# Kernel optimization log

Measured on AMD Instinct MI355X. Metric: run time of the kernel, lower is better.

Reference implementation:

```python
import jax, jax.numpy as jnp
import numpy as np

T, H, E, F = 2048, 1024, 32, 512   # tokens, hidden, routed experts, moe intermediate
K, NG, TG = 8, 8, 4                # top_k, n_group, topk_group
FS = 1024                          # shared-expert intermediate = n_shared(2) * F
SCALE = 2.5                        # routed_scaling_factor


def _silu_and_mul(gu):
    g, u = jnp.split(gu, 2, axis=-1)
    return jax.nn.silu(g) * u


def _route(x, gate_w, bias):
    # DeepSeek-V3 noaux_tc grouped top-k with correction bias (sigmoid scores)
    logits = x @ gate_w.T                                   # [T,E]
    scores = jax.nn.sigmoid(logits.astype(jnp.float32))
    sc = scores + bias[None, :]                             # biased scores, selection only
    n_tok = sc.shape[0]
    grp = sc.reshape(n_tok, NG, E // NG)
    top2, _ = jax.lax.top_k(grp, 2)
    group_scores = top2.sum(-1)                             # [T,NG]
    _, gidx = jax.lax.top_k(group_scores, TG)
    gmask = jnp.zeros((n_tok, NG), scores.dtype).at[jnp.arange(n_tok)[:, None], gidx].set(1.0)
    emask = jnp.repeat(gmask, E // NG, axis=1)              # [T,E]
    masked = jnp.where(emask > 0, sc, -jnp.inf)
    _, topk_idx = jax.lax.top_k(masked, K)                  # [T,K]
    w = jnp.take_along_axis(scores, topk_idx, axis=1)       # unbiased scores as weights
    w = w / (w.sum(-1, keepdims=True) + 1e-20)              # renormalize (norm_topk_prob)
    return w, topk_idx


def _forward(x, gate_w, corr_bias, w_gate_up, w_down, shared_gate_up, shared_down):
    w, idx = _route(x, gate_w, corr_bias)
    # dense grouped-GEMM reference: every expert on every token, sparse combine
    gu = jnp.einsum('th,egh->teg', x, w_gate_up)            # [T,E,2F]
    h = _silu_and_mul(gu)                                   # [T,E,F]
    y = jnp.einsum('tef,ehf->teh', h, w_down)               # [T,E,H]
    n_tok = x.shape[0]
    combine = jnp.zeros((n_tok, E), x.dtype).at[jnp.arange(n_tok)[:, None], idx].add(w.astype(x.dtype))
    routed = jnp.einsum('te,teh->th', combine, y) * SCALE
    shared = _silu_and_mul(x @ shared_gate_up.T) @ shared_down.T
    return routed + shared


def setup_inputs() -> dict:
    key = jax.random.key(0)
    ks = jax.random.split(key, 7)
    return {
        "hidden_states": jax.random.normal(ks[0], (T, H), jnp.float32),
        "gate_w": jax.random.normal(ks[1], (E, H), jnp.float32) * 0.02,
        "corr_bias": jax.random.normal(ks[2], (E,), jnp.float32) * 0.01,
        "w_gate_up": jax.random.normal(ks[3], (E, 2 * F, H), jnp.float32) * 0.02,
        "w_down": jax.random.normal(ks[4], (E, H, F), jnp.float32) * 0.02,
        "shared_gate_up": jax.random.normal(ks[5], (2 * FS, H), jnp.float32) * 0.02,
        "shared_down": jax.random.normal(ks[6], (H, FS), jnp.float32) * 0.02,
        "num_global_tokens": T,
        "max_num_tokens_per_gpu": T,
    }


def reference(hidden_states, gate_w, corr_bias, w_gate_up, w_down, shared_gate_up, shared_down, num_global_tokens, max_num_tokens_per_gpu):
    return _forward(hidden_states, gate_w, corr_bias, w_gate_up, w_down, shared_gate_up, shared_down)
```

## Files before the change

### kernel.cpp

```cpp
#include <hip/hip_runtime.h>
#include <hip/hip_bf16.h>

#define T_TOK 2048
#define H_DIM 1024
#define E_EXP 32
#define F_DIM 512
#define FS_DIM 1024
#define K_TOP 8
#define NGRP 8
#define TGRP 4
#define GSZ (E_EXP / NGRP)
#define RSCALE 2.5f
#define CAP 2048

typedef short  short8 __attribute__((ext_vector_type(8)));
typedef __bf16 bf16x4 __attribute__((ext_vector_type(4)));
typedef __bf16 bf16x8 __attribute__((ext_vector_type(8)));
typedef float  f32x4  __attribute__((ext_vector_type(4)));

#define NROUTE_BLK (T_TOK / 4)
__global__ __launch_bounds__(256) void prep_kernel(
    const float* __restrict__ x, const float* __restrict__ gw,
    const float* __restrict__ bias, int* __restrict__ tk_idx,
    float* __restrict__ tk_w, __bf16* __restrict__ xb,
    const float* __restrict__ s0, __bf16* __restrict__ d0, int n0,
    const float* __restrict__ s1, __bf16* __restrict__ d1, int n1,
    const float* __restrict__ s2, __bf16* __restrict__ d2, int n2,
    const float* __restrict__ s3, __bf16* __restrict__ d3, int n3) {
  if (blockIdx.x < NROUTE_BLK) {
    const int wid = threadIdx.x >> 6, lane = threadIdx.x & 63;
    const int t = blockIdx.x * 4 + wid;
    float xr[16];
#pragma unroll
    for (int i = 0; i < 16; i++) xr[i] = x[t * H_DIM + i * 64 + lane];
#pragma unroll
    for (int i = 0; i < 16; i++) xb[t * H_DIM + i * 64 + lane] = (__bf16)xr[i];
    float sc[E_EXP];
#pragma unroll
    for (int e = 0; e < E_EXP; e++) {
      const float* w = gw + e * H_DIM;
      float s = 0.f;
#pragma unroll
      for (int i = 0; i < 16; i++) s += xr[i] * w[i * 64 + lane];
#pragma unroll
      for (int off = 32; off > 0; off >>= 1) s += __shfl_xor(s, off);
      sc[e] = 1.f / (1.f + expf(-s));
    }
    if (lane == 0) {
      float b[E_EXP];
      for (int e = 0; e < E_EXP; e++) b[e] = sc[e] + bias[e];
      float gs[NGRP];
      for (int g = 0; g < NGRP; g++) {
        float m1 = -1e30f, m2 = -1e30f;
        for (int j = 0; j < GSZ; j++) {
          float v = b[g * GSZ + j];
          if (v > m1) { m2 = m1; m1 = v; } else if (v > m2) { m2 = v; }
        }
        gs[g] = m1 + m2;
      }
      unsigned gmask = 0;
      for (int it = 0; it < TGRP; it++) {
        float best = -1e30f; int bi = 0;
        for (int g = 0; g < NGRP; g++)
          if (!((gmask >> g) & 1) && gs[g] > best) { best = gs[g]; bi = g; }
        gmask |= 1u << bi;
      }
      unsigned emask = 0; float wsum = 0.f;
      int idx8[K_TOP];
      for (int it = 0; it < K_TOP; it++) {
        float best = -1e30f; int bi = 0;
        for (int e = 0; e < E_EXP; e++) {
          if (!((gmask >> (e / GSZ)) & 1)) continue;
          if ((emask >> e) & 1) continue;
          if (b[e] > best) { best = b[e]; bi = e; }
        }
        emask |= 1u << bi;
        idx8[it] = bi;
        wsum += sc[bi];
      }
      const float inv = 1.f / (wsum + 1e-20f);
      for (int k = 0; k < K_TOP; k++) {
        tk_idx[t * K_TOP + k] = idx8[k];
        tk_w[t * K_TOP + k] = sc[idx8[k]] * inv;
      }
    }
  } else {
    const int ntot8 = (n0 + n1 + n2 + n3) >> 1;
    const int nthr = (gridDim.x - NROUTE_BLK) * 256;
    int gid = (blockIdx.x - NROUTE_BLK) * 256 + threadIdx.x;
    for (; gid < ntot8; gid += nthr) {
      int t = gid << 1;
      const float* src; __bf16* dst;
      if (t < n0) { src = s0; dst = d0; }
      else { t -= n0;
        if (t < n1) { src = s1; dst = d1; }
        else { t -= n1;
          if (t < n2) { src = s2; dst = d2; }
          else { t -= n2; src = s3; dst = d3; }
        }
      }
      const float4 va = reinterpret_cast<const float4*>(src)[t];
      const float4 vb = reinterpret_cast<const float4*>(src)[t + 1];
      bf16x8 o;
      o[0] = (__bf16)va.x; o[1] = (__bf16)va.y; o[2] = (__bf16)va.z; o[3] = (__bf16)va.w;
      o[4] = (__bf16)vb.x; o[5] = (__bf16)vb.y; o[6] = (__bf16)vb.z; o[7] = (__bf16)vb.w;
      *reinterpret_cast<bf16x8*>(reinterpret_cast<bf16x4*>(dst) + t) = o;
    }
  }
}

__global__ void scatter_kernel(const int* __restrict__ tk_idx, int* __restrict__ counts,
                               int* __restrict__ recs) {
  const int i = blockIdx.x * blockDim.x + threadIdx.x;
  if (i >= T_TOK * K_TOP) return;
  const int e = tk_idx[i];
  const int pos = atomicAdd(&counts[e], 1);
  recs[e * CAP + pos] = i;
}

#define BM 128
#define BN 128
#define BK 64

__device__ __forceinline__ void gload_lds16(const void* g, void* l) {
  __builtin_amdgcn_global_load_lds(
      (__attribute__((address_space(1))) const void*)g,
      (__attribute__((address_space(3))) void*)l, 16, 0, 0);
}

template <int PHASE>
__global__ __launch_bounds__(256) void gemm_fused(
    const __bf16* __restrict__ Ar, const __bf16* __restrict__ As_,
    const __bf16* __restrict__ Br, const __bf16* __restrict__ Bs_,
    void* __restrict__ OutR, void* __restrict__ OutS,
    const int* __restrict__ recs, const int* __restrict__ counts,
    const float* __restrict__ tk_w) {

  const int z = blockIdx.z;
  const bool routed = (z < E_EXP);
  const int e = z;
  const int m0 = blockIdx.y * BM;
  const int bx = blockIdx.x;

  int count = T_TOK, off_e = 0;
  if (routed) {
    count = counts[e];
    for (int i = 0; i < E_EXP; i++) off_e += (i < e) ? counts[i] : 0;
    if (m0 >= count) return;
  }
  const int K = (PHASE == 0) ? H_DIM : (routed ? F_DIM : FS_DIM);

  const int tid = threadIdx.x, wid = tid >> 6, lane = tid & 63;

  __shared__ __align__(16) __bf16 Atile[BM * BK];
  __shared__ __align__(16) __bf16 Btile[BN * BK];

  const int colk = (lane & 7) * 8;
  const __bf16* aptr[4];
  const __bf16* bptr[4];
#pragma unroll
  for (int i = 0; i < 4; i++) {
    const int row = wid * 32 + i * 8 + (lane >> 3);
    int r = m0 + row; if (r > count - 1) r = count - 1;
    if (PHASE == 0) {
      if (routed) {
        const int rec = recs[e * CAP + r];
        aptr[i] = Ar + (size_t)(rec >> 3) * H_DIM + colk;
      } else {
        aptr[i] = As_ + (size_t)r * H_DIM + colk;
      }
    } else {
      if (routed) aptr[i] = Ar + (size_t)(off_e + r) * F_DIM + colk;
      else        aptr[i] = As_ + (size_t)r * FS_DIM + colk;
    }
    if (PHASE == 0) {
      if (routed) {
        const int brow = (row < 64) ? (bx * 64 + row) : (F_DIM + bx * 64 + row - 64);
        bptr[i] = Br + (size_t)e * 2 * F_DIM * H_DIM + (size_t)brow * H_DIM + colk;
      } else {
        const int s = z - E_EXP;
        const int fglob = s * 512 + bx * 64 + (row & 63);
        const int brow = (row < 64) ? fglob : (FS_DIM + fglob);
        bptr[i] = Bs_ + (size_t)brow * H_DIM + colk;
      }
    } else {
      if (routed) {
        const int brow = bx * BN + row;
        bptr[i] = Br + (size_t)e * H_DIM * F_DIM + (size_t)brow * F_DIM + colk;
      } else {
        const int brow = bx * BN + row;
        bptr[i] = Bs_ + (size_t)brow * FS_DIM + colk;
      }
    }
  }

  f32x4 acc[2][8];
#pragma unroll
  for (int a = 0; a < 2; a++)
#pragma unroll
    for (int b = 0; b < 8; b++) acc[a][b] = f32x4{0.f, 0.f, 0.f, 0.f};

  const int lr = lane & 15, lh = lane >> 4;

  for (int k0 = 0; k0 < K; k0 += BK) {
#pragma unroll
    for (int i = 0; i < 4; i++)
      gload_lds16(aptr[i] + k0, (char*)Atile + (wid * 4 + i) * 1024);
#pragma unroll
    for (int i = 0; i < 4; i++)
      gload_lds16(bptr[i] + k0, (char*)Btile + (wid * 4 + i) * 1024);
    __syncthreads();
#pragma unroll
    for (int kk = 0; kk < 2; kk++) {
      short8 af[2], bfr[8];
#pragma unroll
      for (int fm = 0; fm < 2; fm++)
        af[fm] = *reinterpret_cast<const short8*>(&Atile[(wid * 32 + fm * 16 + lr) * BK + kk * 32 + lh * 8]);
#pragma unroll
      for (int fn = 0; fn < 8; fn++)
        bfr[fn] = *reinterpret_cast<const short8*>(&Btile[(fn * 16 + lr) * BK + kk * 32 + lh * 8]);
#pragma unroll
      for (int fn = 0; fn < 8; fn++)
#pragma unroll
        for (int fm = 0; fm < 2; fm++)
          acc[fm][fn] = __builtin_amdgcn_mfma_f32_16x16x32_bf16(af[fm], bfr[fn], acc[fm][fn], 0, 0, 0);
    }
    __syncthreads();
  }

  if (PHASE == 0) {
#pragma unroll
    for (int fm = 0; fm < 2; fm++)
#pragma unroll
      for (int j = 0; j < 4; j++) {
        const int row = wid * 32 + fm * 16 + lh * 4 + j;
        if (m0 + row < count) {
#pragma unroll
          for (int fn = 0; fn < 4; fn++) {
            const float g = acc[fm][fn][j], u = acc[fm][fn + 4][j];
            const float hv = g / (1.f + expf(-g)) * u;
            if (routed) {
              const int f = bx * 64 + fn * 16 + lr;
              ((__bf16*)OutR)[(size_t)(off_e + m0 + row) * F_DIM + f] = (__bf16)hv;
            } else {
              const int s = z - E_EXP;
              const int f = s * 512 + bx * 64 + fn * 16 + lr;
              ((__bf16*)OutS)[(size_t)(m0 + row) * FS_DIM + f] = (__bf16)hv;
            }
          }
        }
      }
  } else {
#pragma unroll
    for (int fm = 0; fm < 2; fm++)
#pragma unroll
      for (int j = 0; j < 4; j++) {
        const int row = wid * 32 + fm * 16 + lh * 4 + j;
        if (m0 + row < count) {
          if (routed) {
            const int rec = recs[e * CAP + m0 + row];
            const float w = tk_w[rec];
            const size_t base = (size_t)rec * H_DIM + bx * BN;
#pragma unroll
            for (int fn = 0; fn < 8; fn++)
              ((float*)OutR)[base + fn * 16 + lr] = acc[fm][fn][j] * w;
          } else {
#pragma unroll
            for (int fn = 0; fn < 8; fn++)
              ((float*)OutS)[(size_t)(m0 + row) * H_DIM + bx * BN + fn * 16 + lr] = acc[fm][fn][j];
          }
        }
      }
  }
}

__global__ void combine_kernel(const float* __restrict__ y_slot, float* __restrict__ out) {
  const int gid = blockIdx.x * blockDim.x + threadIdx.x;
  const int t = gid >> 8;
  const int c0 = (gid & 255) * 4;
  float4 s = {0.f, 0.f, 0.f, 0.f};
#pragma unroll
  for (int k = 0; k < K_TOP; k++) {
    const float4 v = *reinterpret_cast<const float4*>(&y_slot[((size_t)t * K_TOP + k) * H_DIM + c0]);
    s.x += v.x; s.y += v.y; s.z += v.z; s.w += v.w;
  }
  float4 o = *reinterpret_cast<float4*>(&out[(size_t)t * H_DIM + c0]);
  o.x += RSCALE * s.x; o.y += RSCALE * s.y; o.z += RSCALE * s.z; o.w += RSCALE * s.w;
  *reinterpret_cast<float4*>(&out[(size_t)t * H_DIM + c0]) = o;
}

extern "C" void kernel_launch(void* const* d_in, const int* in_sizes, int n_in,
                              void* d_out, int out_size, void* d_ws, size_t ws_size,
                              hipStream_t stream) {
  const float* x    = (const float*)d_in[0];
  const float* gw   = (const float*)d_in[1];
  const float* bias = (const float*)d_in[2];
  const float* wgu  = (const float*)d_in[3];
  const float* wd   = (const float*)d_in[4];
  const float* sgu  = (const float*)d_in[5];
  const float* sd   = (const float*)d_in[6];

  char* ws = (char*)d_ws;
  size_t o = 0;
  auto alloc = [&](size_t bytes) {
    char* p = ws + o;
    o += (bytes + 255) & ~(size_t)255;
    return (void*)p;
  };
  __bf16* xb     = (__bf16*)alloc((size_t)T_TOK * H_DIM * 2);
  __bf16* wgub   = (__bf16*)alloc((size_t)E_EXP * 2 * F_DIM * H_DIM * 2);
  __bf16* wdb    = (__bf16*)alloc((size_t)E_EXP * H_DIM * F_DIM * 2);
  __bf16* sgub   = (__bf16*)alloc((size_t)2 * FS_DIM * H_DIM * 2);
  __bf16* sdb    = (__bf16*)alloc((size_t)H_DIM * FS_DIM * 2);
  __bf16* h_buf  = (__bf16*)alloc((size_t)T_TOK * K_TOP * F_DIM * 2);
  float*  y_slot = (float*) alloc((size_t)T_TOK * K_TOP * H_DIM * 4);
  __bf16* hs     = (__bf16*)alloc((size_t)T_TOK * FS_DIM * 2);
  int*   tk_idx  = (int*)  alloc((size_t)T_TOK * K_TOP * 4);
  float* tk_w    = (float*)alloc((size_t)T_TOK * K_TOP * 4);
  int*   counts  = (int*)  alloc((size_t)E_EXP * 4);
  int*   recs    = (int*)  alloc((size_t)E_EXP * CAP * 4);
  if (o > ws_size) return;

  hipMemsetAsync(counts, 0, E_EXP * 4, stream);
  prep_kernel<<<2048, 256, 0, stream>>>(
      x, gw, bias, tk_idx, tk_w, xb,
      wgu, wgub, E_EXP * 2 * F_DIM * H_DIM / 4,
      wd,  wdb,  E_EXP * H_DIM * F_DIM / 4,
      sgu, sgub, 2 * FS_DIM * H_DIM / 4,
      sd,  sdb,  H_DIM * FS_DIM / 4);

  scatter_kernel<<<(T_TOK * K_TOP + 255) / 256, 256, 0, stream>>>(tk_idx, counts, recs);

  gemm_fused<0><<<dim3(F_DIM / 64, T_TOK / BM, E_EXP + 2), 256, 0, stream>>>(
      xb, xb, wgub, sgub, h_buf, hs, recs, counts, tk_w);

  gemm_fused<1><<<dim3(H_DIM / BN, T_TOK / BM, E_EXP + 1), 256, 0, stream>>>(
      h_buf, hs, wdb, sdb, y_slot, d_out, recs, counts, tk_w);

  combine_kernel<<<T_TOK * H_DIM / 4 / 256, 256, 0, stream>>>(y_slot, (float*)d_out);
}
```

Before: 290.3 us.

## Overlap down-proj weight conversion with gate-up GEMM via extra grid slices

Moves the fp32-to-bf16 conversion of the routed and shared down-projection weights out of the prep kernel and into extra z-slices of the phase-0 gate/up GEMM launch. The prep kernel then converts only the gate/up weights, and the down-weight conversion runs alongside the GEMM tiles. This is meant to hide part of the bandwidth-bound conversion behind compute-bound GEMM work. In exchange, the two workloads now compete for memory bandwidth and CUs inside the GEMM launch, and the outcome depends on how blocks are scheduled.

```diff
diff --git a/kernel.cpp b/kernel.cpp
--- a/kernel.cpp
+++ b/kernel.cpp
@@ -12,11 +12,30 @@
 #define GSZ (E_EXP / NGRP)
 #define RSCALE 2.5f
 #define CAP 2048
+#define NCVT_SLICE 8
 
 typedef short  short8 __attribute__((ext_vector_type(8)));
 typedef __bf16 bf16x4 __attribute__((ext_vector_type(4)));
 typedef __bf16 bf16x8 __attribute__((ext_vector_type(8)));
 typedef float  f32x4  __attribute__((ext_vector_type(4)));
+
+__device__ __forceinline__ void cvt8_range(const float* __restrict__ s0, __bf16* __restrict__ d0, int n0,
+                                           const float* __restrict__ s1, __bf16* __restrict__ d1, int n1,
+                                           int base, int nthr) {
+  const int ntot8 = (n0 + n1) >> 1;
+  for (int gid = base; gid < ntot8; gid += nthr) {
+    int t = gid << 1;
+    const float* src; __bf16* dst;
+    if (t < n0) { src = s0; dst = d0; }
+    else { t -= n0; src = s1; dst = d1; }
+    const float4 va = reinterpret_cast<const float4*>(src)[t];
+    const float4 vb = reinterpret_cast<const float4*>(src)[t + 1];
+    bf16x8 o;
+    o[0] = (__bf16)va.x; o[1] = (__bf16)va.y; o[2] = (__bf16)va.z; o[3] = (__bf16)va.w;
+    o[4] = (__bf16)vb.x; o[5] = (__bf16)vb.y; o[6] = (__bf16)vb.z; o[7] = (__bf16)vb.w;
+    *reinterpret_cast<bf16x8*>(reinterpret_cast<bf16x4*>(dst) + t) = o;
+  }
+}
 
 #define NROUTE_BLK (T_TOK / 4)
 __global__ __launch_bounds__(256) void prep_kernel(
@@ -24,9 +43,7 @@
     const float* __restrict__ bias, int* __restrict__ tk_idx,
     float* __restrict__ tk_w, __bf16* __restrict__ xb,
     const float* __restrict__ s0, __bf16* __restrict__ d0, int n0,
-    const float* __restrict__ s1, __bf16* __restrict__ d1, int n1,
-    const float* __restrict__ s2, __bf16* __restrict__ d2, int n2,
-    const float* __restrict__ s3, __bf16* __restrict__ d3, int n3) {
+    const float* __restrict__ s1, __bf16* __restrict__ d1, int n1) {
   if (blockIdx.x < NROUTE_BLK) {
     const int wid = threadIdx.x >> 6, lane = threadIdx.x & 63;
     const int t = blockIdx.x * 4 + wid;
@@ -85,27 +102,9 @@
       }
     }
   } else {
-    const int ntot8 = (n0 + n1 + n2 + n3) >> 1;
     const int nthr = (gridDim.x - NROUTE_BLK) * 256;
-    int gid = (blockIdx.x - NROUTE_BLK) * 256 + threadIdx.x;
-    for (; gid < ntot8; gid += nthr) {
-      int t = gid << 1;
-      const float* src; __bf16* dst;
-      if (t < n0) { src = s0; dst = d0; }
-      else { t -= n0;
-        if (t < n1) { src = s1; dst = d1; }
-        else { t -= n1;
-          if (t < n2) { src = s2; dst = d2; }
-          else { t -= n2; src = s3; dst = d3; }
-        }
-      }
-      const float4 va = reinterpret_cast<const float4*>(src)[t];
-      const float4 vb = reinterpret_cast<const float4*>(src)[t + 1];
-      bf16x8 o;
-      o[0] = (__bf16)va.x; o[1] = (__bf16)va.y; o[2] = (__bf16)va.z; o[3] = (__bf16)va.w;
-      o[4] = (__bf16)vb.x; o[5] = (__bf16)vb.y; o[6] = (__bf16)vb.z; o[7] = (__bf16)vb.w;
-      *reinterpret_cast<bf16x8*>(reinterpret_cast<bf16x4*>(dst) + t) = o;
-    }
+    const int base = (blockIdx.x - NROUTE_BLK) * 256 + threadIdx.x;
+    cvt8_range(s0, d0, n0, s1, d1, n1, base, nthr);
   }
 }
 
@@ -134,9 +133,19 @@
     const __bf16* __restrict__ Br, const __bf16* __restrict__ Bs_,
     void* __restrict__ OutR, void* __restrict__ OutS,
     const int* __restrict__ recs, const int* __restrict__ counts,
-    const float* __restrict__ tk_w) {
+    const float* __restrict__ tk_w,
+    const float* __restrict__ cvt_s0, __bf16* __restrict__ cvt_d0, int cvt_n0,
+    const float* __restrict__ cvt_s1, __bf16* __restrict__ cvt_d1, int cvt_n1) {
 
   const int z = blockIdx.z;
+
+  if (PHASE == 0 && z >= E_EXP + 2) {
+    const int nblk = NCVT_SLICE * gridDim.x * gridDim.y;
+    const int bid = (z - (E_EXP + 2)) * gridDim.x * gridDim.y + blockIdx.y * gridDim.x + blockIdx.x;
+    cvt8_range(cvt_s0, cvt_d0, cvt_n0, cvt_s1, cvt_d1, cvt_n1, bid * 256 + threadIdx.x, nblk * 256);
+    return;
+  }
+
   const bool routed = (z < E_EXP);
   const int e = z;
   const int m0 = blockIdx.y * BM;
@@ -325,17 +334,17 @@
   prep_kernel<<<2048, 256, 0, stream>>>(
       x, gw, bias, tk_idx, tk_w, xb,
       wgu, wgub, E_EXP * 2 * F_DIM * H_DIM / 4,
-      wd,  wdb,  E_EXP * H_DIM * F_DIM / 4,
-      sgu, sgub, 2 * FS_DIM * H_DIM / 4,
-      sd,  sdb,  H_DIM * FS_DIM / 4);
+      sgu, sgub, 2 * FS_DIM * H_DIM / 4);
 
   scatter_kernel<<<(T_TOK * K_TOP + 255) / 256, 256, 0, stream>>>(tk_idx, counts, recs);
 
-  gemm_fused<0><<<dim3(F_DIM / 64, T_TOK / BM, E_EXP + 2), 256, 0, stream>>>(
-      xb, xb, wgub, sgub, h_buf, hs, recs, counts, tk_w);
+  gemm_fused<0><<<dim3(F_DIM / 64, T_TOK / BM, E_EXP + 2 + NCVT_SLICE), 256, 0, stream>>>(
+      xb, xb, wgub, sgub, h_buf, hs, recs, counts, tk_w,
+      wd, wdb, E_EXP * H_DIM * F_DIM / 4, sd, sdb, H_DIM * FS_DIM / 4);
 
   gemm_fused<1><<<dim3(H_DIM / BN, T_TOK / BM, E_EXP + 1), 256, 0, stream>>>(
-      h_buf, hs, wdb, sdb, y_slot, d_out, recs, counts, tk_w);
+      h_buf, hs, wdb, sdb, y_slot, d_out, recs, counts, tk_w,
+      (const float*)nullptr, (__bf16*)nullptr, 0, (const float*)nullptr, (__bf16*)nullptr, 0);
 
   combine_kernel<<<T_TOK * H_DIM / 4 / 256, 256, 0, stream>>>(y_slot, (float*)d_out);
 }
```

After: 273.5 us. 1.06x faster.
